# Optimization experiments

Hardware: AMD Instinct MI355X
Metric: run time of the kernel (lower is better)

Reference implementation:

```python
import jax, jax.numpy as jnp
import numpy as np

B, H, W, C = 16, 64, 64, 512
HEADS, WS, SHIFT = 16, 8, 4
N = WS * WS            # tokens per window
HID = 4 * C            # mlp hidden


def _buffers():
    # Swin-V2 log-spaced continuous relative coords table [1, 2ws-1, 2ws-1, 2]
    rc = np.arange(-(WS - 1), WS, dtype=np.float32)
    table = np.stack(np.meshgrid(rc, rc, indexing='ij'), axis=-1)[None]
    table = table / (WS - 1) * 8.0
    table = np.sign(table) * np.log2(np.abs(table) + 1.0) / np.log2(8.0)
    # relative position index [N, N]
    coords = np.stack(np.meshgrid(np.arange(WS), np.arange(WS), indexing='ij')).reshape(2, -1)
    rel = (coords[:, :, None] - coords[:, None, :]).transpose(1, 2, 0)
    rel[..., 0] += WS - 1
    rel[..., 1] += WS - 1
    rel[..., 0] *= 2 * WS - 1
    idx = rel.sum(-1).astype(np.int32)
    # shifted-window attention mask [nW, N, N]
    img = np.zeros((H, W), dtype=np.float32)
    sl = (slice(0, -WS), slice(-WS, -SHIFT), slice(-SHIFT, None))
    cnt = 0
    for hs in sl:
        for ws_ in sl:
            img[hs, ws_] = cnt
            cnt += 1
    mw = img.reshape(H // WS, WS, W // WS, WS).transpose(0, 2, 1, 3).reshape(-1, N)
    am = mw[:, None, :] - mw[:, :, None]
    am = np.where(am != 0, np.float32(-100.0), np.float32(0.0)).astype(np.float32)
    return table.astype(np.float32), idx, am


def setup_inputs() -> dict:
    key = jax.random.key(0)
    ks = jax.random.split(key, 8)
    table, idx, am = _buffers()
    p = lambda k, s: jax.random.normal(k, s, jnp.float32) * 0.02
    return {
        'x': jax.random.normal(ks[0], (B, H * W, C), jnp.float32),
        'qkv_w': p(ks[1], (3 * C, C)),
        'q_bias': jnp.zeros((C,), jnp.float32),
        'v_bias': jnp.zeros((C,), jnp.float32),
        'logit_scale': jnp.full((HEADS, 1, 1), np.log(10.0), jnp.float32),
        'cpb_w1': p(ks[2], (512, 2)),
        'cpb_b1': jnp.zeros((512,), jnp.float32),
        'cpb_w2': p(ks[3], (HEADS, 512)),
        'proj_w': p(ks[4], (C, C)),
        'proj_b': jnp.zeros((C,), jnp.float32),
        'norm1_g': jnp.ones((C,), jnp.float32),
        'norm1_b': jnp.zeros((C,), jnp.float32),
        'norm2_g': jnp.ones((C,), jnp.float32),
        'norm2_b': jnp.zeros((C,), jnp.float32),
        'fc1_w': p(ks[5], (HID, C)),
        'fc1_b': jnp.zeros((HID,), jnp.float32),
        'fc2_w': p(ks[6], (C, HID)),
        'fc2_b': jnp.zeros((C,), jnp.float32),
        'coords_table': jnp.asarray(table),
        'attn_mask': jnp.asarray(am),
        'rel_pos_index': jnp.asarray(idx),
    }


def _layernorm(x, g, b):
    m = x.mean(-1, keepdims=True)
    v = ((x - m) ** 2).mean(-1, keepdims=True)
    return (x - m) / jnp.sqrt(v + 1e-5) * g + b


def reference(x, qkv_w, q_bias, v_bias, logit_scale, cpb_w1, cpb_b1, cpb_w2,
              proj_w, proj_b, norm1_g, norm1_b, norm2_g, norm2_b,
              fc1_w, fc1_b, fc2_w, fc2_b, coords_table, attn_mask, rel_pos_index):
    Bsz, L, Cd = x.shape
    d = Cd // HEADS
    shortcut = x
    # cyclic shift + window partition: [B*nW, N, C]
    xr = jnp.roll(x.reshape(Bsz, H, W, Cd), (-SHIFT, -SHIFT), axis=(1, 2))
    xw = xr.reshape(Bsz, H // WS, WS, W // WS, WS, Cd).transpose(0, 1, 3, 2, 4, 5).reshape(-1, N, Cd)
    B_ = xw.shape[0]
    nW = B_ // Bsz
    # qkv with q/v-only bias
    qkv_bias = jnp.concatenate([q_bias, jnp.zeros_like(v_bias), v_bias])
    qkv = (xw @ qkv_w.T + qkv_bias).reshape(B_, N, 3, HEADS, d).transpose(2, 0, 3, 1, 4)
    q, k, v = qkv[0], qkv[1], qkv[2]  # [B_, h, N, d]
    # cosine attention with learned clamped logit scale
    qn = q / jnp.maximum(jnp.linalg.norm(q, axis=-1, keepdims=True), 1e-12)
    kn = k / jnp.maximum(jnp.linalg.norm(k, axis=-1, keepdims=True), 1e-12)
    scale = jnp.exp(jnp.minimum(logit_scale, jnp.log(jnp.float32(100.0))))
    attn = jnp.einsum('bhnd,bhmd->bhnm', qn, kn) * scale
    # CPB MLP relative position bias
    tbl = jax.nn.relu(coords_table @ cpb_w1.T + cpb_b1) @ cpb_w2.T  # [1,2ws-1,2ws-1,h]
    rpb = tbl.reshape(-1, HEADS)[rel_pos_index.reshape(-1)].reshape(N, N, HEADS).transpose(2, 0, 1)
    attn = attn + 16.0 * jax.nn.sigmoid(rpb)[None]
    # shift mask
    attn = (attn.reshape(Bsz, nW, HEADS, N, N) + attn_mask[None, :, None]).reshape(B_, HEADS, N, N)
    attn = jax.nn.softmax(attn, axis=-1)
    out = jnp.einsum('bhnm,bhmd->bhnd', attn, v).transpose(0, 2, 1, 3).reshape(B_, N, Cd)
    out = out @ proj_w.T + proj_b
    # window reverse + reverse shift
    out = out.reshape(Bsz, H // WS, W // WS, WS, WS, Cd).transpose(0, 1, 3, 2, 4, 5).reshape(Bsz, H, W, Cd)
    out = jnp.roll(out, (SHIFT, SHIFT), axis=(1, 2)).reshape(Bsz, L, Cd)
    # Swin-V2 post-norm residuals
    x1 = shortcut + _layernorm(out, norm1_g, norm1_b)
    mlp = jax.nn.gelu(x1 @ fc1_w.T + fc1_b, approximate=False) @ fc2_w.T + fc2_b
    return x1 + _layernorm(mlp, norm2_g, norm2_b)
```

## Files before the change

kernel.cpp:

```cpp
#include <hip/hip_runtime.h>
#include <hip/hip_bf16.h>
#include <math.h>

#define BB     16
#define HH     64
#define WWID   64
#define CCH    512
#define HEADS  16
#define NTOK   64
#define DDIM   32
#define NWIN   64
#define LL     (HH*WWID)
#define MTOT   (BB*LL)
#define BWIN   (BB*NWIN)
#define HIDN   2048
#define SHIFT_ 4

typedef unsigned short u16;
using bf16x8 = __attribute__((ext_vector_type(8))) short;
using f32x4  = __attribute__((ext_vector_type(4))) float;

__device__ __forceinline__ u16 f2bf(float f) {
  union { float f; unsigned u; } v; v.f = f;
  unsigned r = v.u + 0x7fffu + ((v.u >> 16) & 1u);
  return (u16)(r >> 16);
}
__device__ __forceinline__ float bf2f(unsigned h) {
  union { unsigned u; float f; } v; v.u = h << 16;
  return v.f;
}
__device__ __forceinline__ unsigned cvtpk(float lo, float hi) {
  unsigned r;
  asm("v_cvt_pk_bf16_f32 %0, %1, %2" : "=v"(r) : "v"(lo), "v"(hi));
  return r;
}
__device__ __forceinline__ float gelu_f(float v) {
  float v3 = v * v * v;
  float y = 1.5957691216057308f * v + 0.0713548162726009f * v3;
  return v / (1.f + __expf(-y));
}

__device__ __forceinline__ void gload16(const void* g, void* l) {
  __builtin_amdgcn_global_load_lds((const __attribute__((address_space(1))) void*)g,
                                   (__attribute__((address_space(3))) void*)l, 16, 0, 0);
}

__device__ __forceinline__ int win2orig(int b_, int n) {
  int b = b_ >> 6, wi = b_ & 63;
  int hs = (wi >> 3) * 8 + (n >> 3);
  int ws = (wi & 7) * 8 + (n & 7);
  int hq = (hs + SHIFT_) & 63;
  int wq = (ws + SHIFT_) & 63;
  return b * LL + hq * WWID + wq;
}

__global__ void cvt_k(const float* __restrict__ s, u16* __restrict__ d, int n) {
  int i = blockIdx.x * 256 + threadIdx.x;
  if (i < n) d[i] = f2bf(s[i]);
}

__global__ void cpb_k(const float* __restrict__ ct, const float* __restrict__ w1,
                      const float* __restrict__ b1, const float* __restrict__ w2,
                      float* __restrict__ t2) {
  int t = blockIdx.x * 256 + threadIdx.x;
  if (t >= 225 * 16) return;
  int rr = t >> 4, h = t & 15;
  float c0 = ct[rr * 2], c1 = ct[rr * 2 + 1];
  float acc = 0.f;
  for (int j = 0; j < 512; j++) {
    float hv = fmaxf(w1[j * 2] * c0 + w1[j * 2 + 1] * c1 + b1[j], 0.f);
    acc += hv * w2[h * 512 + j];
  }
  t2[t] = acc;
}

__global__ void bias_k(const float* __restrict__ t2, const int* __restrict__ rpi,
                       float* __restrict__ b16) {
  int t = blockIdx.x * 256 + threadIdx.x;
  int nm = t & 4095;
  int h = t >> 12;
  float v = t2[rpi[nm] * 16 + h];
  b16[t] = 16.0f / (1.0f + __expf(-v));
}

__global__ void scale_k(const float* __restrict__ ls, float* __restrict__ sc) {
  int t = threadIdx.x;
  if (t < HEADS) sc[t] = __expf(fminf(ls[t], 4.6051701859880914f));
}

__global__ __launch_bounds__(256) void xw_k(const float* __restrict__ x, u16* __restrict__ xw) {
  int t = blockIdx.x * 256 + threadIdx.x;
  int row = t >> 6;
  int col = (t & 63) * 8;
  const float* src = x + (size_t)win2orig(row >> 6, row & 63) * CCH + col;
  float4 a = *(const float4*)src;
  float4 b = *(const float4*)(src + 4);
  uint4 o = make_uint4(cvtpk(a.x, a.y), cvtpk(a.z, a.w),
                       cvtpk(b.x, b.y), cvtpk(b.z, b.w));
  *(uint4*)(xw + (size_t)row * CCH + col) = o;
}

template<int MODE, int NBN>
__global__ __launch_bounds__(512, 2) void gemm256_k(
    const u16* __restrict__ A, const u16* __restrict__ Bw,
    const float* __restrict__ bias,
    const float* __restrict__ qbias, const float* __restrict__ vbias,
    u16* __restrict__ o0, u16* __restrict__ o1, u16* __restrict__ o2,
    int K, int mchunk)
{
  __shared__ __align__(16) u16 smem[2 * 32768];
  const int t = threadIdx.x;
  const int lin = blockIdx.x;
  const int xcd = lin & 7;
  const int j = lin >> 3;
  const int m0 = (xcd * mchunk + j / NBN) * 256;
  const int n0 = (j % NBN) * 256;
  const int lane = t & 63;
  const int wv = t >> 6;
  const int wr = wv >> 2;
  const int wc = wv & 3;
  const int l15 = lane & 15;
  const int l4 = lane >> 4;

  const int rl = t >> 3;
  const int cg = (t & 7) ^ ((t >> 3) & 7);
  const int ck0 = (l4) ^ (lane & 7);
  const int ck1 = (4 + l4) ^ (lane & 7);

  auto stageU = [&](int T, int u, int bi) {
    const u16* mat = (u < 2) ? A : Bw;
    const int gbase = ((u < 2) ? m0 : n0) + (u & 1) * 128;
    size_t roff = (size_t)(gbase + rl) * K + (size_t)T * 64 + cg * 8;
    char* lds = (char*)smem + bi * 65536 + (u >= 2 ? 32768 : 0) + (u & 1) * 16384 + wv * 1024;
    gload16(mat + roff, lds);
    gload16(mat + roff + (size_t)64 * K, lds + 8192);
  };

  f32x4 acc[8][4] = {};

  const int NT = K >> 6;
  #pragma unroll
  for (int u = 0; u < 4; u++) stageU(0, u, 0);
  asm volatile("s_waitcnt vmcnt(0)" ::: "memory");
  __builtin_amdgcn_s_barrier();

  for (int it = 0; it < NT; ++it) {
    const int cur = it & 1, nxt = cur ^ 1;
    const u16* bufA = smem + cur * 32768;
    const u16* bufB = bufA + 16384;
    const bool st = (it + 1 < NT);
    bf16x8 bfr[4];

    {
      bf16x8 afr[4];
      #pragma unroll
      for (int nf = 0; nf < 4; nf++)
        bfr[nf] = *(const bf16x8*)&bufB[(wc * 64 + nf * 16 + l15) * 64 + ck0 * 8];
      #pragma unroll
      for (int fm = 0; fm < 4; fm++)
        afr[fm] = *(const bf16x8*)&bufA[(wr * 128 + fm * 16 + l15) * 64 + ck0 * 8];
      if (st) { stageU(it + 1, 0, nxt); stageU(it + 1, 1, nxt); }
      __builtin_amdgcn_s_barrier();
      asm volatile("s_waitcnt lgkmcnt(0)" ::: "memory");
      __builtin_amdgcn_sched_barrier(0);
      __builtin_amdgcn_s_setprio(1);
      #pragma unroll
      for (int fm = 0; fm < 4; fm++)
        #pragma unroll
        for (int nf = 0; nf < 4; nf++)
          acc[fm][nf] = __builtin_amdgcn_mfma_f32_16x16x32_bf16(bfr[nf], afr[fm], acc[fm][nf], 0, 0, 0);
      __builtin_amdgcn_s_setprio(0);
      __builtin_amdgcn_s_barrier();
    }
    {
      bf16x8 afr[4];
      #pragma unroll
      for (int fm = 0; fm < 4; fm++)
        afr[fm] = *(const bf16x8*)&bufA[(wr * 128 + 64 + fm * 16 + l15) * 64 + ck0 * 8];
      if (st) { stageU(it + 1, 2, nxt); stageU(it + 1, 3, nxt); }
      __builtin_amdgcn_s_barrier();
      asm volatile("s_waitcnt lgkmcnt(0)" ::: "memory");
      __builtin_amdgcn_sched_barrier(0);
      __builtin_amdgcn_s_setprio(1);
      #pragma unroll
      for (int fm = 0; fm < 4; fm++)
        #pragma unroll
        for (int nf = 0; nf < 4; nf++)
          acc[4 + fm][nf] = __builtin_amdgcn_mfma_f32_16x16x32_bf16(bfr[nf], afr[fm], acc[4 + fm][nf], 0, 0, 0);
      __builtin_amdgcn_s_setprio(0);
      __builtin_amdgcn_s_barrier();
    }
    {
      bf16x8 afr[4];
      #pragma unroll
      for (int nf = 0; nf < 4; nf++)
        bfr[nf] = *(const bf16x8*)&bufB[(wc * 64 + nf * 16 + l15) * 64 + ck1 * 8];
      #pragma unroll
      for (int fm = 0; fm < 4; fm++)
        afr[fm] = *(const bf16x8*)&bufA[(wr * 128 + fm * 16 + l15) * 64 + ck1 * 8];
      __builtin_amdgcn_s_barrier();
      asm volatile("s_waitcnt lgkmcnt(0)" ::: "memory");
      __builtin_amdgcn_sched_barrier(0);
      __builtin_amdgcn_s_setprio(1);
      #pragma unroll
      for (int fm = 0; fm < 4; fm++)
        #pragma unroll
        for (int nf = 0; nf < 4; nf++)
          acc[fm][nf] = __builtin_amdgcn_mfma_f32_16x16x32_bf16(bfr[nf], afr[fm], acc[fm][nf], 0, 0, 0);
      __builtin_amdgcn_s_setprio(0);
      __builtin_amdgcn_s_barrier();
    }
    {
      bf16x8 afr[4];
      #pragma unroll
      for (int fm = 0; fm < 4; fm++)
        afr[fm] = *(const bf16x8*)&bufA[(wr * 128 + 64 + fm * 16 + l15) * 64 + ck1 * 8];
      __builtin_amdgcn_s_barrier();
      asm volatile("s_waitcnt lgkmcnt(0)" ::: "memory");
      __builtin_amdgcn_sched_barrier(0);
      __builtin_amdgcn_s_setprio(1);
      #pragma unroll
      for (int fm = 0; fm < 4; fm++)
        #pragma unroll
        for (int nf = 0; nf < 4; nf++)
          acc[4 + fm][nf] = __builtin_amdgcn_mfma_f32_16x16x32_bf16(bfr[nf], afr[fm], acc[4 + fm][nf], 0, 0, 0);
      __builtin_amdgcn_s_setprio(0);
      asm volatile("s_waitcnt vmcnt(0)" ::: "memory");
      __builtin_amdgcn_s_barrier();
    }
  }

  const int part = n0 >> 9;
  u16* qkvdst = (MODE == 0) ? (part == 0 ? o0 : (part == 1 ? o1 : o2)) : o0;
  const int l4q = l4 * 4;
  #pragma unroll
  for (int mf = 0; mf < 8; mf++) {
    const int grow = m0 + wr * 128 + mf * 16 + l15;
    size_t rowbase;
    if (MODE == 0) {
      int b_ = grow >> 6, n = grow & 63;
      rowbase = ((size_t)b_ * HEADS) * (NTOK * DDIM) + (size_t)n * DDIM;
    } else if (MODE == 1) {
      rowbase = (size_t)win2orig(grow >> 6, grow & 63) * CCH;
    } else if (MODE == 2) {
      rowbase = (size_t)grow * HIDN;
    } else {
      rowbase = (size_t)grow * CCH;
    }
    #pragma unroll
    for (int nf = 0; nf < 4; nf++) {
      const int n = n0 + wc * 64 + nf * 16 + l4q;
      float v0 = acc[mf][nf][0];
      float v1 = acc[mf][nf][1];
      float v2 = acc[mf][nf][2];
      float v3 = acc[mf][nf][3];
      if (MODE == 0) {
        const int cc = n & 511;
        if (part == 0) {
          float4 b4 = *(const float4*)(qbias + cc);
          v0 += b4.x; v1 += b4.y; v2 += b4.z; v3 += b4.w;
        } else if (part == 2) {
          float4 b4 = *(const float4*)(vbias + cc);
          v0 += b4.x; v1 += b4.y; v2 += b4.z; v3 += b4.w;
        }
      } else {
        float4 b4 = *(const float4*)(bias + n);
        v0 += b4.x; v1 += b4.y; v2 += b4.z; v3 += b4.w;
        if (MODE == 2) {
          v0 = gelu_f(v0); v1 = gelu_f(v1); v2 = gelu_f(v2); v3 = gelu_f(v3);
        }
      }
      uint2 pk = make_uint2(cvtpk(v0, v1), cvtpk(v2, v3));
      if (MODE == 0) {
        const int cc = n & 511;
        const int hh = cc >> 5, dd = cc & 31;
        *(uint2*)(qkvdst + rowbase + (size_t)hh * (NTOK * DDIM) + dd) = pk;
      } else {
        *(uint2*)(o0 + rowbase + n) = pk;
      }
    }
  }
}

__global__ __launch_bounds__(64) void attn_k(
    const u16* __restrict__ qb, const u16* __restrict__ kb, const u16* __restrict__ vb,
    const float* __restrict__ bias16, const float* __restrict__ scale,
    const float* __restrict__ amask, u16* __restrict__ attn_out)
{
  __shared__ u16 Pmat[64][72];
  __shared__ u16 vT[32][72];

  int bh = blockIdx.x;
  int b_ = bh >> 4, h = bh & 15;
  int wi = b_ & 63;
  int lane = threadIdx.x;
  int l15 = lane & 15, quad = lane >> 4;
  const u16* qs = qb + (size_t)bh * (NTOK * DDIM);
  const u16* ks = kb + (size_t)bh * (NTOK * DDIM);
  const u16* vs = vb + (size_t)bh * (NTOK * DDIM);

  bf16x8 qf[4], kf[4];
  #pragma unroll
  for (int mt = 0; mt < 4; mt++) {
    qf[mt] = *(const bf16x8*)(qs + (mt * 16 + l15) * DDIM + quad * 8);
    kf[mt] = *(const bf16x8*)(ks + (mt * 16 + l15) * DDIM + quad * 8);
  }
  #pragma unroll
  for (int mt = 0; mt < 4; mt++) {
    float sq = 0.f, sk = 0.f;
    #pragma unroll
    for (int jj = 0; jj < 8; jj++) {
      float a = bf2f((u16)qf[mt][jj]); sq += a * a;
      float b = bf2f((u16)kf[mt][jj]); sk += b * b;
    }
    sq += __shfl_xor(sq, 16); sq += __shfl_xor(sq, 32);
    sk += __shfl_xor(sk, 16); sk += __shfl_xor(sk, 32);
    float iq = 1.f / fmaxf(sqrtf(sq), 1e-12f);
    float ik = 1.f / fmaxf(sqrtf(sk), 1e-12f);
    #pragma unroll
    for (int jj = 0; jj < 8; jj++) {
      qf[mt][jj] = (short)f2bf(bf2f((u16)qf[mt][jj]) * iq);
      kf[mt][jj] = (short)f2bf(bf2f((u16)kf[mt][jj]) * ik);
    }
  }
  f32x4 s[4][4];
  #pragma unroll
  for (int mt = 0; mt < 4; mt++)
    #pragma unroll
    for (int nt = 0; nt < 4; nt++) {
      f32x4 c = {0.f, 0.f, 0.f, 0.f};
      s[mt][nt] = __builtin_amdgcn_mfma_f32_16x16x32_bf16(qf[mt], kf[nt], c, 0, 0, 0);
    }
  #pragma unroll
  for (int d8 = 0; d8 < 4; d8++) {
    bf16x8 vv = *(const bf16x8*)(vs + lane * DDIM + d8 * 8);
    #pragma unroll
    for (int jj = 0; jj < 8; jj++) vT[d8 * 8 + jj][lane] = (u16)vv[jj];
  }

  float sc = scale[h];
  float rinv[4][4];
  const float* bbase = bias16 + (size_t)h * 4096;
  const float* mbase = amask + (size_t)wi * 4096;
  #pragma unroll
  for (int mt = 0; mt < 4; mt++) {
    #pragma unroll
    for (int i = 0; i < 4; i++) {
      int row = mt * 16 + quad * 4 + i;
      const float* bro = bbase + row * 64;
      const float* mro = mbase + row * 64;
      float p[4];
      float mx = -1e30f;
      #pragma unroll
      for (int nt = 0; nt < 4; nt++) {
        int col = nt * 16 + l15;
        float vv = s[mt][nt][i] * sc + bro[col] + mro[col];
        p[nt] = vv;
        mx = fmaxf(mx, vv);
      }
      mx = fmaxf(mx, __shfl_xor(mx, 1));
      mx = fmaxf(mx, __shfl_xor(mx, 2));
      mx = fmaxf(mx, __shfl_xor(mx, 4));
      mx = fmaxf(mx, __shfl_xor(mx, 8));
      float sum = 0.f;
      #pragma unroll
      for (int nt = 0; nt < 4; nt++) {
        float e = __expf(p[nt] - mx);
        p[nt] = e;
        sum += e;
      }
      sum += __shfl_xor(sum, 1);
      sum += __shfl_xor(sum, 2);
      sum += __shfl_xor(sum, 4);
      sum += __shfl_xor(sum, 8);
      rinv[mt][i] = 1.f / sum;
      #pragma unroll
      for (int nt = 0; nt < 4; nt++)
        Pmat[row][nt * 16 + l15] = f2bf(p[nt]);
    }
  }
  __syncthreads();

  f32x4 oacc[4][2] = {};
  #pragma unroll
  for (int ks2 = 0; ks2 < 2; ks2++) {
    bf16x8 pf[4], vf[2];
    #pragma unroll
    for (int mt = 0; mt < 4; mt++)
      pf[mt] = *(const bf16x8*)&Pmat[mt * 16 + l15][ks2 * 32 + quad * 8];
    #pragma unroll
    for (int nt = 0; nt < 2; nt++)
      vf[nt] = *(const bf16x8*)&vT[nt * 16 + l15][ks2 * 32 + quad * 8];
    #pragma unroll
    for (int mt = 0; mt < 4; mt++)
      #pragma unroll
      for (int nt = 0; nt < 2; nt++)
        oacc[mt][nt] = __builtin_amdgcn_mfma_f32_16x16x32_bf16(pf[mt], vf[nt], oacc[mt][nt], 0, 0, 0);
  }
  #pragma unroll
  for (int mt = 0; mt < 4; mt++)
    #pragma unroll
    for (int nt = 0; nt < 2; nt++)
      #pragma unroll
      for (int i = 0; i < 4; i++) {
        int n = mt * 16 + quad * 4 + i;
        int d = nt * 16 + l15;
        float val = oacc[mt][nt][i] * rinv[mt][i];
        attn_out[(size_t)(b_ * 64 + n) * CCH + h * DDIM + d] = f2bf(val);
      }
}

__global__ __launch_bounds__(256) void ln_res_k(
    const float* __restrict__ xin, const u16* __restrict__ pin,
    const float* __restrict__ gam, const float* __restrict__ bet,
    float* __restrict__ x1f, u16* __restrict__ x1b)
{
  int row = blockIdx.x * 4 + (threadIdx.x >> 6);
  int lane = threadIdx.x & 63;
  size_t base = (size_t)row * CCH + lane * 8;
  uint4 u = *(const uint4*)(pin + base);
  unsigned w[4] = {u.x, u.y, u.z, u.w};
  float pv[8];
  #pragma unroll
  for (int j = 0; j < 4; j++) {
    pv[j * 2] = bf2f(w[j] & 0xffffu);
    pv[j * 2 + 1] = bf2f(w[j] >> 16);
  }
  float4 x0 = *(const float4*)(xin + base);
  float4 x1 = *(const float4*)(xin + base + 4);
  float xr[8] = {x0.x, x0.y, x0.z, x0.w, x1.x, x1.y, x1.z, x1.w};
  float s = 0.f, sq = 0.f;
  #pragma unroll
  for (int j = 0; j < 8; j++) { s += pv[j]; sq += pv[j] * pv[j]; }
  #pragma unroll
  for (int o = 32; o > 0; o >>= 1) { s += __shfl_xor(s, o, 64); sq += __shfl_xor(sq, o, 64); }
  float mean = s * (1.0f / 512.0f);
  float var = sq * (1.0f / 512.0f) - mean * mean;
  float rstd = rsqrtf(var + 1e-5f);
  float4 g0 = *(const float4*)(gam + lane * 8);
  float4 g1 = *(const float4*)(gam + lane * 8 + 4);
  float4 b0 = *(const float4*)(bet + lane * 8);
  float4 b1 = *(const float4*)(bet + lane * 8 + 4);
  float gg[8] = {g0.x, g0.y, g0.z, g0.w, g1.x, g1.y, g1.z, g1.w};
  float bb[8] = {b0.x, b0.y, b0.z, b0.w, b1.x, b1.y, b1.z, b1.w};
  float val[8];
  #pragma unroll
  for (int j = 0; j < 8; j++)
    val[j] = xr[j] + (pv[j] - mean) * rstd * gg[j] + bb[j];
  *(float4*)(x1f + base)     = make_float4(val[0], val[1], val[2], val[3]);
  *(float4*)(x1f + base + 4) = make_float4(val[4], val[5], val[6], val[7]);
  *(uint4*)(x1b + base) = make_uint4(cvtpk(val[0], val[1]), cvtpk(val[2], val[3]),
                                     cvtpk(val[4], val[5]), cvtpk(val[6], val[7]));
}

__global__ __launch_bounds__(256) void ln_fin_k(
    const u16* __restrict__ mlp, const float* __restrict__ gam,
    const float* __restrict__ bet, float* __restrict__ io)
{
  int row = blockIdx.x * 4 + (threadIdx.x >> 6);
  int lane = threadIdx.x & 63;
  size_t base = (size_t)row * CCH + lane * 8;
  uint4 u = *(const uint4*)(mlp + base);
  unsigned w[4] = {u.x, u.y, u.z, u.w};
  float pv[8];
  #pragma unroll
  for (int j = 0; j < 4; j++) {
    pv[j * 2] = bf2f(w[j] & 0xffffu);
    pv[j * 2 + 1] = bf2f(w[j] >> 16);
  }
  float s = 0.f, sq = 0.f;
  #pragma unroll
  for (int j = 0; j < 8; j++) { s += pv[j]; sq += pv[j] * pv[j]; }
  #pragma unroll
  for (int o = 32; o > 0; o >>= 1) { s += __shfl_xor(s, o, 64); sq += __shfl_xor(sq, o, 64); }
  float mean = s * (1.0f / 512.0f);
  float var = sq * (1.0f / 512.0f) - mean * mean;
  float rstd = rsqrtf(var + 1e-5f);
  float4 g0 = *(const float4*)(gam + lane * 8);
  float4 g1 = *(const float4*)(gam + lane * 8 + 4);
  float4 b0 = *(const float4*)(bet + lane * 8);
  float4 b1 = *(const float4*)(bet + lane * 8 + 4);
  float gg[8] = {g0.x, g0.y, g0.z, g0.w, g1.x, g1.y, g1.z, g1.w};
  float bb[8] = {b0.x, b0.y, b0.z, b0.w, b1.x, b1.y, b1.z, b1.w};
  float4 i0 = *(const float4*)(io + base);
  float4 i1 = *(const float4*)(io + base + 4);
  float iv[8] = {i0.x, i0.y, i0.z, i0.w, i1.x, i1.y, i1.z, i1.w};
  float out[8];
  #pragma unroll
  for (int j = 0; j < 8; j++)
    out[j] = iv[j] + (pv[j] - mean) * rstd * gg[j] + bb[j];
  *(float4*)(io + base)     = make_float4(out[0], out[1], out[2], out[3]);
  *(float4*)(io + base + 4) = make_float4(out[4], out[5], out[6], out[7]);
}

#define OFF_Q     ((size_t)0)
#define OFF_K     ((size_t)67108864)
#define OFF_V     ((size_t)134217728)
#define OFF_ATTN  ((size_t)201326592)
#define OFF_X1B   ((size_t)268435456)
#define OFF_WQKV  ((size_t)335544320)
#define OFF_WPROJ ((size_t)337117184)
#define OFF_WFC1  ((size_t)337641472)
#define OFF_WFC2  ((size_t)339738624)
#define OFF_T2    ((size_t)341835776)
#define OFF_B16   ((size_t)341852160)
#define OFF_SC    ((size_t)342114304)

extern "C" void kernel_launch(void* const* d_in, const int* in_sizes, int n_in,
                              void* d_out, int out_size, void* d_ws, size_t ws_size,
                              hipStream_t stream) {
  const float* x        = (const float*)d_in[0];
  const float* qkv_w    = (const float*)d_in[1];
  const float* q_bias   = (const float*)d_in[2];
  const float* v_bias   = (const float*)d_in[3];
  const float* lscale   = (const float*)d_in[4];
  const float* cpb_w1   = (const float*)d_in[5];
  const float* cpb_b1   = (const float*)d_in[6];
  const float* cpb_w2   = (const float*)d_in[7];
  const float* proj_w   = (const float*)d_in[8];
  const float* proj_b   = (const float*)d_in[9];
  const float* n1g      = (const float*)d_in[10];
  const float* n1b      = (const float*)d_in[11];
  const float* n2g      = (const float*)d_in[12];
  const float* n2b      = (const float*)d_in[13];
  const float* fc1_w    = (const float*)d_in[14];
  const float* fc1_b    = (const float*)d_in[15];
  const float* fc2_w    = (const float*)d_in[16];
  const float* fc2_b    = (const float*)d_in[17];
  const float* ctab     = (const float*)d_in[18];
  const float* amask    = (const float*)d_in[19];
  const int*   rpi      = (const int*)d_in[20];

  char* ws = (char*)d_ws;
  float* outp = (float*)d_out;

  u16*   q_buf    = (u16*)(ws + OFF_Q);
  u16*   k_buf    = (u16*)(ws + OFF_K);
  u16*   v_buf    = (u16*)(ws + OFF_V);
  u16*   proj_out = (u16*)(ws + OFF_Q);
  u16*   hid      = (u16*)(ws + OFF_Q);
  u16*   xw       = (u16*)(ws + OFF_ATTN);
  u16*   attn_out = (u16*)(ws + OFF_ATTN);
  u16*   mlp_out  = (u16*)(ws + OFF_ATTN);
  u16*   x1b      = (u16*)(ws + OFF_X1B);
  u16*   wqkv     = (u16*)(ws + OFF_WQKV);
  u16*   wproj    = (u16*)(ws + OFF_WPROJ);
  u16*   wfc1     = (u16*)(ws + OFF_WFC1);
  u16*   wfc2     = (u16*)(ws + OFF_WFC2);
  float* t2       = (float*)(ws + OFF_T2);
  float* b16      = (float*)(ws + OFF_B16);
  float* scbuf    = (float*)(ws + OFF_SC);

  cvt_k<<<(1536 * 512 + 255) / 256, 256, 0, stream>>>(qkv_w, wqkv, 1536 * 512);
  cvt_k<<<(512 * 512 + 255) / 256, 256, 0, stream>>>(proj_w, wproj, 512 * 512);
  cvt_k<<<(2048 * 512 + 255) / 256, 256, 0, stream>>>(fc1_w, wfc1, 2048 * 512);
  cvt_k<<<(512 * 2048 + 255) / 256, 256, 0, stream>>>(fc2_w, wfc2, 512 * 2048);
  cpb_k<<<15, 256, 0, stream>>>(ctab, cpb_w1, cpb_b1, cpb_w2, t2);
  bias_k<<<256, 256, 0, stream>>>(t2, rpi, b16);
  scale_k<<<1, 64, 0, stream>>>(lscale, scbuf);

  xw_k<<<MTOT * 64 / 256, 256, 0, stream>>>(x, xw);
  gemm256_k<0, 6><<<256 * 6, 512, 0, stream>>>(
      xw, wqkv, nullptr, q_bias, v_bias, q_buf, k_buf, v_buf, 512, 32);
  attn_k<<<BWIN * HEADS, 64, 0, stream>>>(q_buf, k_buf, v_buf, b16, scbuf, amask, attn_out);
  gemm256_k<1, 2><<<256 * 2, 512, 0, stream>>>(
      attn_out, wproj, proj_b, nullptr, nullptr, proj_out, nullptr, nullptr, 512, 32);
  ln_res_k<<<MTOT / 4, 256, 0, stream>>>(x, proj_out, n1g, n1b, outp, x1b);
  for (int half = 0; half < 2; half++) {
    const u16* a1 = x1b + (size_t)half * (MTOT / 2) * CCH;
    u16* m1 = mlp_out + (size_t)half * (MTOT / 2) * CCH;
    gemm256_k<2, 8><<<128 * 8, 512, 0, stream>>>(
        a1, wfc1, fc1_b, nullptr, nullptr, hid, nullptr, nullptr, 512, 16);
    gemm256_k<3, 2><<<128 * 2, 512, 0, stream>>>(
        hid, wfc2, fc2_b, nullptr, nullptr, m1, nullptr, nullptr, 2048, 16);
  }
  ln_fin_k<<<MTOT / 4, 256, 0, stream>>>(mlp_out, n2g, n2b, outp);
}
```

Baseline: 1.041 ms.

## Switch GEMM to triple-buffered K=32 tiles with two-stage prefetch

```diff
diff --git a/kernel.cpp b/kernel.cpp
--- a/kernel.cpp
+++ b/kernel.cpp
@@ -101,14 +101,14 @@
 }
 
 template<int MODE, int NBN>
-__global__ __launch_bounds__(512, 2) void gemm256_k(
+__global__ __launch_bounds__(512, 1) void gemm256_k(
     const u16* __restrict__ A, const u16* __restrict__ Bw,
     const float* __restrict__ bias,
     const float* __restrict__ qbias, const float* __restrict__ vbias,
     u16* __restrict__ o0, u16* __restrict__ o1, u16* __restrict__ o2,
     int K, int mchunk)
 {
-  __shared__ __align__(16) u16 smem[2 * 32768];
+  __shared__ __align__(16) u16 smem[3 * 16384];
   const int t = threadIdx.x;
   const int lin = blockIdx.x;
   const int xcd = lin & 7;
@@ -122,44 +122,51 @@
   const int l15 = lane & 15;
   const int l4 = lane >> 4;
 
-  const int rl = t >> 3;
-  const int cg = (t & 7) ^ ((t >> 3) & 7);
-  const int ck0 = (l4) ^ (lane & 7);
-  const int ck1 = (4 + l4) ^ (lane & 7);
-
-  auto stageU = [&](int T, int u, int bi) {
-    const u16* mat = (u < 2) ? A : Bw;
-    const int gbase = ((u < 2) ? m0 : n0) + (u & 1) * 128;
-    size_t roff = (size_t)(gbase + rl) * K + (size_t)T * 64 + cg * 8;
-    char* lds = (char*)smem + bi * 65536 + (u >= 2 ? 32768 : 0) + (u & 1) * 16384 + wv * 1024;
-    gload16(mat + roff, lds);
-    gload16(mat + roff + (size_t)64 * K, lds + 8192);
+  const int swcol = (((t & 3) ^ ((t >> 2) & 3)) * 8);
+  const u16* aP[2]; const u16* bP[2];
+  #pragma unroll
+  for (int i = 0; i < 2; i++) {
+    aP[i] = A  + (size_t)(m0 + i * 128 + (t >> 2)) * K + swcol;
+    bP[i] = Bw + (size_t)(n0 + i * 128 + (t >> 2)) * K + swcol;
+  }
+  const int ck = l4 ^ (lane & 3);
+
+  auto stageA = [&](int k0, int bi) {
+    char* base = (char*)smem + bi * 32768;
+    gload16(aP[0] + k0, base + wv * 1024);
+    gload16(aP[1] + k0, base + 8192 + wv * 1024);
   };
+  auto stageB = [&](int k0, int bi) {
+    char* base = (char*)smem + bi * 32768 + 16384;
+    gload16(bP[0] + k0, base + wv * 1024);
+    gload16(bP[1] + k0, base + 8192 + wv * 1024);
+  };
 
   f32x4 acc[8][4] = {};
 
-  const int NT = K >> 6;
-  #pragma unroll
-  for (int u = 0; u < 4; u++) stageU(0, u, 0);
-  asm volatile("s_waitcnt vmcnt(0)" ::: "memory");
+  const int NT = K >> 5;
+  stageA(0, 0);  stageB(0, 0);
+  stageA(32, 1); stageB(32, 1);
+  asm volatile("s_waitcnt vmcnt(4)" ::: "memory");
   __builtin_amdgcn_s_barrier();
 
   for (int it = 0; it < NT; ++it) {
-    const int cur = it & 1, nxt = cur ^ 1;
-    const u16* bufA = smem + cur * 32768;
-    const u16* bufB = bufA + 16384;
-    const bool st = (it + 1 < NT);
+    const int bi = it % 3;
+    const u16* bufA = smem + bi * 16384;
+    const u16* bufB = bufA + 8192;
+    const bool st = (it + 2 < NT);
+    const int kp = (it + 2) << 5;
     bf16x8 bfr[4];
 
     {
       bf16x8 afr[4];
       #pragma unroll
       for (int nf = 0; nf < 4; nf++)
-        bfr[nf] = *(const bf16x8*)&bufB[(wc * 64 + nf * 16 + l15) * 64 + ck0 * 8];
+        bfr[nf] = *(const bf16x8*)&bufB[(wc * 64 + nf * 16 + l15) * 32 + ck * 8];
       #pragma unroll
       for (int fm = 0; fm < 4; fm++)
-        afr[fm] = *(const bf16x8*)&bufA[(wr * 128 + fm * 16 + l15) * 64 + ck0 * 8];
-      if (st) { stageU(it + 1, 0, nxt); stageU(it + 1, 1, nxt); }
+        afr[fm] = *(const bf16x8*)&bufA[(wr * 128 + fm * 16 + l15) * 32 + ck * 8];
+      if (st) stageA(kp, (it + 2) % 3);
       __builtin_amdgcn_s_barrier();
       asm volatile("s_waitcnt lgkmcnt(0)" ::: "memory");
       __builtin_amdgcn_sched_barrier(0);
@@ -176,8 +183,8 @@
       bf16x8 afr[4];
       #pragma unroll
       for (int fm = 0; fm < 4; fm++)
-        afr[fm] = *(const bf16x8*)&bufA[(wr * 128 + 64 + fm * 16 + l15) * 64 + ck0 * 8];
-      if (st) { stageU(it + 1, 2, nxt); stageU(it + 1, 3, nxt); }
+        afr[fm] = *(const bf16x8*)&bufA[(wr * 128 + 64 + fm * 16 + l15) * 32 + ck * 8];
+      if (st) stageB(kp, (it + 2) % 3);
       __builtin_amdgcn_s_barrier();
       asm volatile("s_waitcnt lgkmcnt(0)" ::: "memory");
       __builtin_amdgcn_sched_barrier(0);
@@ -188,44 +195,10 @@
         for (int nf = 0; nf < 4; nf++)
           acc[4 + fm][nf] = __builtin_amdgcn_mfma_f32_16x16x32_bf16(bfr[nf], afr[fm], acc[4 + fm][nf], 0, 0, 0);
       __builtin_amdgcn_s_setprio(0);
-      __builtin_amdgcn_s_barrier();
-    }
-    {
-      bf16x8 afr[4];
-      #pragma unroll
-      for (int nf = 0; nf < 4; nf++)
-        bfr[nf] = *(const bf16x8*)&bufB[(wc * 64 + nf * 16 + l15) * 64 + ck1 * 8];
-      #pragma unroll
-      for (int fm = 0; fm < 4; fm++)
-        afr[fm] = *(const bf16x8*)&bufA[(wr * 128 + fm * 16 + l15) * 64 + ck1 * 8];
-      __builtin_amdgcn_s_barrier();
-      asm volatile("s_waitcnt lgkmcnt(0)" ::: "memory");
-      __builtin_amdgcn_sched_barrier(0);
-      __builtin_amdgcn_s_setprio(1);
-      #pragma unroll
-      for (int fm = 0; fm < 4; fm++)
-        #pragma unroll
-        for (int nf = 0; nf < 4; nf++)
-          acc[fm][nf] = __builtin_amdgcn_mfma_f32_16x16x32_bf16(bfr[nf], afr[fm], acc[fm][nf], 0, 0, 0);
-      __builtin_amdgcn_s_setprio(0);
-      __builtin_amdgcn_s_barrier();
-    }
-    {
-      bf16x8 afr[4];
-      #pragma unroll
-      for (int fm = 0; fm < 4; fm++)
-        afr[fm] = *(const bf16x8*)&bufA[(wr * 128 + 64 + fm * 16 + l15) * 64 + ck1 * 8];
-      __builtin_amdgcn_s_barrier();
-      asm volatile("s_waitcnt lgkmcnt(0)" ::: "memory");
-      __builtin_amdgcn_sched_barrier(0);
-      __builtin_amdgcn_s_setprio(1);
-      #pragma unroll
-      for (int fm = 0; fm < 4; fm++)
-        #pragma unroll
-        for (int nf = 0; nf < 4; nf++)
-          acc[4 + fm][nf] = __builtin_amdgcn_mfma_f32_16x16x32_bf16(bfr[nf], afr[fm], acc[4 + fm][nf], 0, 0, 0);
-      __builtin_amdgcn_s_setprio(0);
-      asm volatile("s_waitcnt vmcnt(0)" ::: "memory");
+      if (it + 1 < NT) {
+        if (st) asm volatile("s_waitcnt vmcnt(4)" ::: "memory");
+        else    asm volatile("s_waitcnt vmcnt(0)" ::: "memory");
+      }
       __builtin_amdgcn_s_barrier();
     }
   }
```

New measurement: 1.089 ms. 1.05x slower.
